# Kernel tuning notes

Hardware: AMD Instinct MI355X
Metric: run time of the kernel (lower is better)

## Reference

```python
import jax, jax.numpy as jnp
import numpy as np

N_HEADS = 16
HEAD_DIM = 128
ROPE_DIM = 64
ROPE_BASE = 10000.0


def _rope(x, base):
    # x: (B, H, S, dim) -- standard rotate-half RoPE, positions = arange(S)
    B, H, S, dim = x.shape
    inv_freq = 1.0 / (base ** (jnp.arange(0, dim, 2, dtype=jnp.float32) / dim))
    pos = jnp.arange(S, dtype=jnp.float32)
    freqs = pos[:, None] * inv_freq[None, :]                  # (S, dim/2)
    emb = jnp.concatenate([freqs, freqs], axis=-1)            # (S, dim)
    cos = jnp.cos(emb).astype(x.dtype)[None, None]
    sin = jnp.sin(emb).astype(x.dtype)[None, None]
    x1, x2 = x[..., : dim // 2], x[..., dim // 2 :]
    rot = jnp.concatenate([-x2, x1], axis=-1)
    return x * cos + rot * sin


def setup_inputs() -> dict:
    key = jax.random.key(0)
    ks = jax.random.split(key, 7)
    B, S, D = 2, 2048, 2048
    s = 0.02
    return {
        "x": jax.random.normal(ks[0], (B, S, D), jnp.float32),
        "Wq": jax.random.normal(ks[1], (D, N_HEADS * HEAD_DIM), jnp.float32) * s,
        "Wq_rope": jax.random.normal(ks[2], (D, N_HEADS * ROPE_DIM), jnp.float32) * s,
        "Wkv_down": jax.random.normal(ks[3], (D, 512), jnp.float32) * s,
        "Wkv_up": jax.random.normal(ks[4], (512, 2 * N_HEADS * HEAD_DIM), jnp.float32) * s,
        "Wk_rope": jax.random.normal(ks[5], (D, ROPE_DIM), jnp.float32) * s,
        "Wo": jax.random.normal(ks[6], (D, D), jnp.float32) * s,
    }


def reference(x, Wq, Wq_rope, Wkv_down, Wkv_up, Wk_rope, Wo):
    B, S, D = x.shape
    H, hd, rd = N_HEADS, HEAD_DIM, ROPE_DIM

    # content and decoupled-RoPE queries
    q_c = (x @ Wq).reshape(B, S, H, hd).transpose(0, 2, 1, 3)        # (B,H,S,hd)
    q_r = (x @ Wq_rope).reshape(B, S, H, rd).transpose(0, 2, 1, 3)   # (B,H,S,rd)
    q_r = _rope(q_r, ROPE_BASE)

    # low-rank KV latent + shared rope key
    c_kv = x @ Wkv_down                                              # (B,S,r)
    k_r = _rope((x @ Wk_rope)[:, None, :, :], ROPE_BASE)             # (B,1,S,rd)

    kv = c_kv @ Wkv_up                                               # (B,S,2*H*hd)
    k_c, v = jnp.split(kv, 2, axis=-1)
    k_c = k_c.reshape(B, S, H, hd).transpose(0, 2, 1, 3)             # (B,H,S,hd)
    v = v.reshape(B, S, H, hd).transpose(0, 2, 1, 3)                 # (B,H,S,hd)

    q_full = jnp.concatenate([q_c, q_r], axis=-1)                    # (B,H,S,hd+rd)
    k_full = jnp.concatenate([k_c, jnp.broadcast_to(k_r, (B, H, S, rd))], axis=-1)

    scale = 1.0 / np.sqrt(hd + rd).astype(np.float32)
    scores = jnp.einsum("bhqd,bhkd->bhqk", q_full, k_full) * scale   # (B,H,S,S)
    mask = jnp.tril(jnp.ones((S, S), dtype=bool))
    scores = jnp.where(mask[None, None], scores, jnp.finfo(scores.dtype).min)
    attn = jax.nn.softmax(scores, axis=-1)

    out = jnp.einsum("bhqk,bhkd->bhqd", attn, v)                     # (B,H,S,hd)
    out = out.transpose(0, 2, 1, 3).reshape(B, S, D)
    return out @ Wo
```

## Files before the change

kernel.cpp:

```cpp
#include <hip/hip_runtime.h>
#include <hip/hip_bf16.h>
#include <cstdint>
#include <cstddef>

typedef unsigned short u16;
typedef __attribute__((ext_vector_type(8))) short short8;
typedef __attribute__((ext_vector_type(4))) float f32x4;
typedef __attribute__((ext_vector_type(16))) float f32x16;

__device__ __forceinline__ u16 f2bf(float f) {
    union { float f; uint32_t u; } v; v.f = f;
    uint32_t u = v.u;
    return (u16)((u + 0x7fffu + ((u >> 16) & 1u)) >> 16);
}
__device__ __forceinline__ float bf2f(u16 u) {
    union { uint32_t u; float f; } v; v.u = ((uint32_t)u) << 16;
    return v.f;
}
__device__ __forceinline__ uint32_t pk2(float lo, float hi) {
    return (uint32_t)f2bf(lo) | ((uint32_t)f2bf(hi) << 16);
}

__device__ __forceinline__ void async_cp16(const u16* g, u16* l) {
    __builtin_amdgcn_global_load_lds(
        (const __attribute__((address_space(1))) unsigned int*)g,
        (__attribute__((address_space(3))) unsigned int*)l, 16, 0, 0);
}

__global__ __launch_bounds__(256) void cast_f32_bf16(const float* __restrict__ in,
                                                     u16* __restrict__ out, int n) {
    int i = (blockIdx.x * 256 + threadIdx.x) * 4;
    if (i >= n) return;
    float4 v = *(const float4*)(in + i);
    ushort4 r;
    r.x = f2bf(v.x); r.y = f2bf(v.y); r.z = f2bf(v.z); r.w = f2bf(v.w);
    *(ushort4*)(out + i) = r;
}

__global__ __launch_bounds__(256) void transpose_cast(const float* __restrict__ W,
                                                      u16* __restrict__ Wt, int K, int N,
                                                      float smul) {
    __shared__ u16 tile[64][72];
    int kt = blockIdx.x * 64, nt = blockIdx.y * 64;
    int t = threadIdx.x;
#pragma unroll
    for (int i = 0; i < 16; i++) {
        int idx = t + i * 256; int kl = idx >> 6, nl = idx & 63;
        tile[kl][nl] = f2bf(W[(size_t)(kt + kl) * N + nt + nl] * smul);
    }
    __syncthreads();
#pragma unroll
    for (int i = 0; i < 16; i++) {
        int idx = t + i * 256; int nl = idx >> 6, kl = idx & 63;
        Wt[(size_t)(nt + nl) * K + kt + kl] = tile[kl][nl];
    }
}

template <int OUTF32, int KDIM, int NDIM>
__global__ __launch_bounds__(256) void gemm_bt(const u16* __restrict__ A, int lda,
                                               const u16* __restrict__ Bt,
                                               void* __restrict__ Cout, int ldc) {
    __shared__ __align__(16) u16 Al[128 * 32];
    __shared__ __align__(16) u16 Bl[128 * 32];
    int m0 = blockIdx.x * 128, n0 = blockIdx.y * 128;
    int t = threadIdx.x;
    int w = t >> 6, l = t & 63;
    int lm = l & 15, lq = l >> 4;
    int wm = (w >> 1) * 64, wn = (w & 1) * 64;
    f32x4 acc[4][4] = {};

    for (int k0 = 0; k0 < KDIM; k0 += 32) {
#pragma unroll
        for (int c = 0; c < 2; c++) {
            int chunk = w * 128 + c * 64 + l;
            int row = chunk >> 2, col8 = (chunk & 3) * 8;
            async_cp16(A + (size_t)(m0 + row) * lda + k0 + col8,
                       Al + (w * 128 + c * 64) * 8);
            int brow = n0 + row;
            if (NDIM % 128 != 0) { if (brow >= NDIM) brow = NDIM - 1; }
            async_cp16(Bt + (size_t)brow * KDIM + k0 + col8,
                       Bl + (w * 128 + c * 64) * 8);
        }
        __syncthreads();
        short8 af[4], bfr[4];
#pragma unroll
        for (int mt = 0; mt < 4; mt++)
            af[mt] = *(const short8*)(Al + (wm + mt * 16 + lm) * 32 + lq * 8);
#pragma unroll
        for (int nt = 0; nt < 4; nt++)
            bfr[nt] = *(const short8*)(Bl + (wn + nt * 16 + lm) * 32 + lq * 8);
#pragma unroll
        for (int mt = 0; mt < 4; mt++)
#pragma unroll
            for (int nt = 0; nt < 4; nt++)
                acc[mt][nt] = __builtin_amdgcn_mfma_f32_16x16x32_bf16(af[mt], bfr[nt], acc[mt][nt], 0, 0, 0);
        __syncthreads();
    }
#pragma unroll
    for (int mt = 0; mt < 4; mt++) {
#pragma unroll
        for (int nt = 0; nt < 4; nt++) {
            int col = n0 + wn + nt * 16 + lm;
            if (col < NDIM) {
#pragma unroll
                for (int r = 0; r < 4; r++) {
                    int row = m0 + wm + mt * 16 + lq * 4 + r;
                    if (OUTF32) ((float*)Cout)[(size_t)row * ldc + col] = acc[mt][nt][r];
                    else        ((u16*)Cout)[(size_t)row * ldc + col] = f2bf(acc[mt][nt][r]);
                }
            }
        }
    }
}

__global__ __launch_bounds__(256) void rope_kernel(u16* __restrict__ x, int rows,
                                                   int nheads, int Smask, int stride) {
    int i = blockIdx.x * 256 + threadIdx.x;
    int total = rows * nheads * 32;
    if (i >= total) return;
    int j = i & 31;
    int h = (i >> 5) % nheads;
    int row = i / (32 * nheads);
    int pos = row & Smask;
    float f = exp2f((float)j * -0.4152410118609828f);
    float ang = (float)pos * f;
    float c = cosf(ang), s = sinf(ang);
    u16* p = x + (size_t)row * stride + h * 64 + j;
    float x1 = bf2f(p[0]), x2 = bf2f(p[32]);
    p[0]  = f2bf(x1 * c - x2 * s);
    p[32] = f2bf(x2 * c + x1 * s);
}

__global__ __launch_bounds__(256) void transpose_v(const u16* __restrict__ kv,
                                                   u16* __restrict__ vt, int S) {
    __shared__ u16 tile[64][72];
    int bh = blockIdx.z; int b = bh >> 4, h = bh & 15;
    int s0 = blockIdx.x * 64, d0 = blockIdx.y * 64;
    int t = threadIdx.x;
#pragma unroll
    for (int i = 0; i < 16; i++) {
        int idx = t + i * 256; int sl = idx >> 6, dl = idx & 63;
        tile[sl][dl] = kv[(size_t)(b * S + s0 + sl) * 4096 + 2048 + h * 128 + d0 + dl];
    }
    __syncthreads();
#pragma unroll
    for (int i = 0; i < 16; i++) {
        int idx = t + i * 256; int dl = idx >> 6, sl = idx & 63;
        vt[((size_t)(bh * 128 + d0 + dl)) * S + s0 + sl] = tile[sl][dl];
    }
}

__global__ __launch_bounds__(256, 2) void mla_attn(const u16* __restrict__ qc, int qcs,
                                                   const u16* __restrict__ qr, int qrs,
                                                   const u16* __restrict__ kvbuf,
                                                   const u16* __restrict__ kr, int krs,
                                                   const u16* __restrict__ vt,
                                                   u16* __restrict__ out, int S) {
    __shared__ __align__(16) u16 Kl[64 * 200];
    __shared__ __align__(16) u16 Vl[128 * 72];
    const float NEG = -1e30f;
    int bh = blockIdx.x; int b = bh >> 4, h = bh & 15;
    int y = blockIdx.y;
    int qt = (y < 8) ? (15 - y) : (y - 8);
    int t = threadIdx.x, w = t >> 6, l = t & 63;
    int ln = l & 31, hi = l >> 5;

    short8 kreg[6], vreg[4];
    auto load_tile = [&](int kbase) {
#pragma unroll
        for (int c = 0; c < 6; c++) {
            int idx = t + c * 256;
            int row = idx / 24, col = (idx % 24) * 8;
            const u16* src = (col < 128)
                ? kvbuf + (size_t)(b * S + kbase + row) * 4096 + h * 128 + col
                : kr + (size_t)(b * S + kbase + row) * krs + (col - 128);
            kreg[c] = *(const short8*)src;
        }
#pragma unroll
        for (int c = 0; c < 4; c++) {
            int idx = t + c * 256;
            int row = idx >> 3, col = (idx & 7) * 8;
            vreg[c] = *(const short8*)(vt + ((size_t)bh * 128 + row) * S + kbase + col);
        }
    };

    int qrow = qt * 128 + w * 32;
    int ntiles = 2 * qt + 2;

    short8 bq[12];
    {
        const u16* qc_row = qc + (size_t)(b * S + qrow + ln) * qcs + h * 128;
#pragma unroll
        for (int ks = 0; ks < 8; ks++) bq[ks] = *(const short8*)(qc_row + ks * 16 + hi * 8);
        const u16* qr_row = qr + (size_t)(b * S + qrow + ln) * qrs + h * 64;
#pragma unroll
        for (int ks = 0; ks < 4; ks++) bq[8 + ks] = *(const short8*)(qr_row + ks * 16 + hi * 8);
    }

    f32x16 o[4] = {};
    float m_s = 0.0f, l_s = 0.f;

    load_tile(0);
    for (int kt = 0; kt < ntiles; kt++) {
        int kbase = kt * 64;
        __syncthreads();
#pragma unroll
        for (int c = 0; c < 6; c++) {
            int idx = t + c * 256;
            int row = idx / 24, col = (idx % 24) * 8;
            *(short8*)(Kl + row * 200 + col) = kreg[c];
        }
#pragma unroll
        for (int c = 0; c < 4; c++) {
            int idx = t + c * 256;
            int row = idx >> 3, col = (idx & 7) * 8;
            *(short8*)(Vl + row * 72 + col) = vreg[c];
        }
        __syncthreads();
        if (kt + 1 < ntiles) load_tile(kbase + 64);

        if (kbase > qrow + 31) continue;

        f32x16 sacc[2] = {};
        __builtin_amdgcn_s_setprio(1);
#pragma unroll
        for (int ks = 0; ks < 12; ks++) {
            short8 ak0 = *(const short8*)(Kl + ln * 200 + ks * 16 + hi * 8);
            short8 ak1 = *(const short8*)(Kl + (32 + ln) * 200 + ks * 16 + hi * 8);
            sacc[0] = __builtin_amdgcn_mfma_f32_32x32x16_bf16(ak0, bq[ks], sacc[0], 0, 0, 0);
            sacc[1] = __builtin_amdgcn_mfma_f32_32x32x16_bf16(ak1, bq[ks], sacc[1], 0, 0, 0);
        }
        __builtin_amdgcn_s_setprio(0);

        if (kbase + 63 > qrow) {
            int qi = qrow + ln;
#pragma unroll
            for (int kt2 = 0; kt2 < 2; kt2++)
#pragma unroll
                for (int r = 0; r < 16; r++) {
                    int key = kbase + kt2 * 32 + (r & 3) + 8 * (r >> 2) + 4 * hi;
                    if (key > qi) sacc[kt2][r] = NEG;
                }
        }

        float mx = NEG;
#pragma unroll
        for (int kt2 = 0; kt2 < 2; kt2++)
#pragma unroll
            for (int r = 0; r < 16; r++) mx = fmaxf(mx, sacc[kt2][r]);
        mx = fmaxf(mx, __shfl_xor(mx, 32));
        if (!__all(mx - m_s <= 8.0f)) {
            float mnew = fmaxf(m_s, mx);
            float alpha = exp2f(m_s - mnew);
            m_s = mnew;
            l_s *= alpha;
#pragma unroll
            for (int dt = 0; dt < 4; dt++) o[dt] *= alpha;
        }

        float rs = 0.f;
        short8 bp[2][2];
#pragma unroll
        for (int kt2 = 0; kt2 < 2; kt2++) {
            float p[16];
#pragma unroll
            for (int r = 0; r < 16; r++) p[r] = exp2f(sacc[kt2][r] - m_s);
#pragma unroll
            for (int r = 0; r < 16; r++) rs += p[r];
            uint32_t c0 = pk2(p[0], p[1]),  c1 = pk2(p[2], p[3]);
            uint32_t c2 = pk2(p[4], p[5]),  c3 = pk2(p[6], p[7]);
            uint32_t e0 = __shfl_xor(c0, 32), e1 = __shfl_xor(c1, 32);
            uint32_t e2 = __shfl_xor(c2, 32), e3 = __shfl_xor(c3, 32);
            union { uint32_t u[4]; short8 s; } f0;
            f0.u[0] = hi ? e2 : c0;
            f0.u[1] = hi ? e3 : c1;
            f0.u[2] = hi ? c2 : e0;
            f0.u[3] = hi ? c3 : e1;
            bp[kt2][0] = f0.s;
            uint32_t c4 = pk2(p[8], p[9]),   c5 = pk2(p[10], p[11]);
            uint32_t c6 = pk2(p[12], p[13]), c7 = pk2(p[14], p[15]);
            uint32_t e4 = __shfl_xor(c4, 32), e5 = __shfl_xor(c5, 32);
            uint32_t e6 = __shfl_xor(c6, 32), e7 = __shfl_xor(c7, 32);
            union { uint32_t u[4]; short8 s; } f1;
            f1.u[0] = hi ? e6 : c4;
            f1.u[1] = hi ? e7 : c5;
            f1.u[2] = hi ? c6 : e4;
            f1.u[3] = hi ? c7 : e5;
            bp[kt2][1] = f1.s;
        }
        rs += __shfl_xor(rs, 32);
        l_s += rs;

        __builtin_amdgcn_s_setprio(1);
#pragma unroll
        for (int kt2 = 0; kt2 < 2; kt2++)
#pragma unroll
            for (int s = 0; s < 2; s++)
#pragma unroll
                for (int dt = 0; dt < 4; dt++) {
                    short8 av = *(const short8*)(Vl + (dt * 32 + ln) * 72 + kt2 * 32 + s * 16 + hi * 8);
                    o[dt] = __builtin_amdgcn_mfma_f32_32x32x16_bf16(av, bp[kt2][s], o[dt], 0, 0, 0);
                }
        __builtin_amdgcn_s_setprio(0);
    }

    float inv = 1.0f / l_s;
    u16* orow = out + (size_t)(b * S + qrow + ln) * 2048 + h * 128;
#pragma unroll
    for (int dt = 0; dt < 4; dt++)
#pragma unroll
        for (int g = 0; g < 4; g++) {
            ushort4 pk4;
            pk4.x = f2bf(o[dt][g * 4 + 0] * inv);
            pk4.y = f2bf(o[dt][g * 4 + 1] * inv);
            pk4.z = f2bf(o[dt][g * 4 + 2] * inv);
            pk4.w = f2bf(o[dt][g * 4 + 3] * inv);
            *(ushort4*)(orow + dt * 32 + g * 8 + hi * 4) = pk4;
        }
}

extern "C" void kernel_launch(void* const* d_in, const int* in_sizes, int n_in,
                              void* d_out, int out_size, void* d_ws, size_t ws_size,
                              hipStream_t stream) {
    const int B = 2, S = 2048, D = 2048, H = 16;
    const int M = B * S;
    const int NP = 3648;
    const int NPpad = 3712;
    const float scale = 0.07216878364870323f * 1.4426950408889634f;
    const float* x    = (const float*)d_in[0];
    const float* Wq   = (const float*)d_in[1];
    const float* Wqr  = (const float*)d_in[2];
    const float* Wkvd = (const float*)d_in[3];
    const float* Wkvu = (const float*)d_in[4];
    const float* Wkr  = (const float*)d_in[5];
    const float* Wo   = (const float*)d_in[6];

    u16* p = (u16*)d_ws;
    u16* xb     = p; p += (size_t)M * D;
    u16* WprojT = p; p += (size_t)NPpad * 2048;
    u16* WkvuT  = p; p += (size_t)4096 * 512;
    u16* WoT    = p; p += (size_t)2048 * 2048;
    u16* proj   = p; p += (size_t)M * NPpad;
    u16* kv     = p; p += (size_t)M * 4096;
    u16* v_t    = p; p += (size_t)B * H * 128 * S;
    u16* attn   = p; p += (size_t)M * 2048;

    u16* q_c = proj;
    u16* q_r = proj + 2048;
    u16* ckv = proj + 3072;
    u16* k_r = proj + 3584;

    cast_f32_bf16<<<(M * D) / 4 / 256, 256, 0, stream>>>(x, xb, M * D);
    transpose_cast<<<dim3(32, 32), 256, 0, stream>>>(Wq,   WprojT,               2048, 2048, scale);
    transpose_cast<<<dim3(32, 16), 256, 0, stream>>>(Wqr,  WprojT + 2048 * 2048, 2048, 1024, scale);
    transpose_cast<<<dim3(32, 8),  256, 0, stream>>>(Wkvd, WprojT + 3072 * 2048, 2048, 512, 1.0f);
    transpose_cast<<<dim3(32, 1),  256, 0, stream>>>(Wkr,  WprojT + 3584 * 2048, 2048, 64, 1.0f);
    transpose_cast<<<dim3(8, 64),  256, 0, stream>>>(Wkvu, WkvuT, 512, 4096, 1.0f);
    transpose_cast<<<dim3(32, 32), 256, 0, stream>>>(Wo,   WoT,   2048, 2048, 1.0f);

    gemm_bt<0, 2048, NP><<<dim3(32, 29), 256, 0, stream>>>(xb, 2048, WprojT, proj, NPpad);

    rope_kernel<<<(M * 16 * 32) / 256, 256, 0, stream>>>(q_r, M, 16, S - 1, NPpad);
    rope_kernel<<<(M * 32) / 256, 256, 0, stream>>>(k_r, M, 1, S - 1, NPpad);

    gemm_bt<0, 512, 4096><<<dim3(32, 32), 256, 0, stream>>>(ckv, NPpad, WkvuT, kv, 4096);
    transpose_v<<<dim3(32, 2, 32), 256, 0, stream>>>(kv, v_t, S);

    mla_attn<<<dim3(32, 16), 256, 0, stream>>>(q_c, NPpad, q_r, NPpad, kv, k_r, NPpad,
                                               v_t, attn, S);

    gemm_bt<1, 2048, 2048><<<dim3(32, 16), 256, 0, stream>>>(attn, 2048, WoT, d_out, 2048);
}
```

Measured before the change: 418.6 us.

## Load K and V fragments directly from global memory, dropping LDS staging

The attention kernel no longer stages K/V tiles through shared memory with register prefetch and block barriers. Each wave now reads its MFMA operands straight from global memory and runs only as many key tiles as its own causal range needs. The query-tile ordering is also simplified to plain descending order. This removes the LDS writes and the __syncthreads, but the four waves in a block no longer share K/V loads, which multiplies global/L2 traffic and exposes load latency because there is no prefetch.

```diff
diff --git a/kernel.cpp b/kernel.cpp
--- a/kernel.cpp
+++ b/kernel.cpp
@@ -156,36 +156,14 @@
                                                    const u16* __restrict__ kr, int krs,
                                                    const u16* __restrict__ vt,
                                                    u16* __restrict__ out, int S) {
-    __shared__ __align__(16) u16 Kl[64 * 200];
-    __shared__ __align__(16) u16 Vl[128 * 72];
     const float NEG = -1e30f;
     int bh = blockIdx.x; int b = bh >> 4, h = bh & 15;
-    int y = blockIdx.y;
-    int qt = (y < 8) ? (15 - y) : (y - 8);
+    int qt = 15 - (int)blockIdx.y;
     int t = threadIdx.x, w = t >> 6, l = t & 63;
     int ln = l & 31, hi = l >> 5;
 
-    short8 kreg[6], vreg[4];
-    auto load_tile = [&](int kbase) {
-#pragma unroll
-        for (int c = 0; c < 6; c++) {
-            int idx = t + c * 256;
-            int row = idx / 24, col = (idx % 24) * 8;
-            const u16* src = (col < 128)
-                ? kvbuf + (size_t)(b * S + kbase + row) * 4096 + h * 128 + col
-                : kr + (size_t)(b * S + kbase + row) * krs + (col - 128);
-            kreg[c] = *(const short8*)src;
-        }
-#pragma unroll
-        for (int c = 0; c < 4; c++) {
-            int idx = t + c * 256;
-            int row = idx >> 3, col = (idx & 7) * 8;
-            vreg[c] = *(const short8*)(vt + ((size_t)bh * 128 + row) * S + kbase + col);
-        }
-    };
-
     int qrow = qt * 128 + w * 32;
-    int ntiles = 2 * qt + 2;
+    int nt_w = (qrow + 31) / 64 + 1;
 
     short8 bq[12];
     {
@@ -200,33 +178,26 @@
     f32x16 o[4] = {};
     float m_s = 0.0f, l_s = 0.f;
 
-    load_tile(0);
-    for (int kt = 0; kt < ntiles; kt++) {
+    for (int kt = 0; kt < nt_w; kt++) {
         int kbase = kt * 64;
-        __syncthreads();
-#pragma unroll
-        for (int c = 0; c < 6; c++) {
-            int idx = t + c * 256;
-            int row = idx / 24, col = (idx % 24) * 8;
-            *(short8*)(Kl + row * 200 + col) = kreg[c];
-        }
-#pragma unroll
-        for (int c = 0; c < 4; c++) {
-            int idx = t + c * 256;
-            int row = idx >> 3, col = (idx & 7) * 8;
-            *(short8*)(Vl + row * 72 + col) = vreg[c];
-        }
-        __syncthreads();
-        if (kt + 1 < ntiles) load_tile(kbase + 64);
-
-        if (kbase > qrow + 31) continue;
-
+
+        const u16* k0p = kvbuf + (size_t)(b * S + kbase + ln) * 4096 + h * 128;
+        const u16* k1p = k0p + (size_t)32 * 4096;
+        const u16* r0p = kr + (size_t)(b * S + kbase + ln) * krs;
+        const u16* r1p = r0p + (size_t)32 * krs;
         f32x16 sacc[2] = {};
         __builtin_amdgcn_s_setprio(1);
 #pragma unroll
-        for (int ks = 0; ks < 12; ks++) {
-            short8 ak0 = *(const short8*)(Kl + ln * 200 + ks * 16 + hi * 8);
-            short8 ak1 = *(const short8*)(Kl + (32 + ln) * 200 + ks * 16 + hi * 8);
+        for (int ks = 0; ks < 8; ks++) {
+            short8 ak0 = *(const short8*)(k0p + ks * 16 + hi * 8);
+            short8 ak1 = *(const short8*)(k1p + ks * 16 + hi * 8);
+            sacc[0] = __builtin_amdgcn_mfma_f32_32x32x16_bf16(ak0, bq[ks], sacc[0], 0, 0, 0);
+            sacc[1] = __builtin_amdgcn_mfma_f32_32x32x16_bf16(ak1, bq[ks], sacc[1], 0, 0, 0);
+        }
+#pragma unroll
+        for (int ks = 8; ks < 12; ks++) {
+            short8 ak0 = *(const short8*)(r0p + (ks - 8) * 16 + hi * 8);
+            short8 ak1 = *(const short8*)(r1p + (ks - 8) * 16 + hi * 8);
             sacc[0] = __builtin_amdgcn_mfma_f32_32x32x16_bf16(ak0, bq[ks], sacc[0], 0, 0, 0);
             sacc[1] = __builtin_amdgcn_mfma_f32_32x32x16_bf16(ak1, bq[ks], sacc[1], 0, 0, 0);
         }
@@ -291,6 +262,7 @@
         rs += __shfl_xor(rs, 32);
         l_s += rs;
 
+        const u16* vb = vt + ((size_t)bh * 128 + ln) * S + kbase;
         __builtin_amdgcn_s_setprio(1);
 #pragma unroll
         for (int kt2 = 0; kt2 < 2; kt2++)
@@ -298,7 +270,7 @@
             for (int s = 0; s < 2; s++)
 #pragma unroll
                 for (int dt = 0; dt < 4; dt++) {
-                    short8 av = *(const short8*)(Vl + (dt * 32 + ln) * 72 + kt2 * 32 + s * 16 + hi * 8);
+                    short8 av = *(const short8*)(vb + (size_t)(dt * 32) * S + kt2 * 32 + s * 16 + hi * 8);
                     o[dt] = __builtin_amdgcn_mfma_f32_32x32x16_bf16(av, bp[kt2][s], o[dt], 0, 0, 0);
                 }
         __builtin_amdgcn_s_setprio(0);
```

Measured after the change: 572.4 us. 1.37x slower.
